# Kernel optimization log

Measured on AMD Instinct MI355X. Metric: run time of the kernel, lower is better.

Reference implementation:

```python
import jax, jax.numpy as jnp
import numpy as np

EPS = 1e-12  # guard sqrt at zero distance


def setup_inputs() -> dict:
    key = jax.random.key(0)
    k1, k2 = jax.random.split(key)
    B, C, N = 4, 3, 8192
    predict_pc = jax.random.normal(k1, (B, C, N), dtype=jnp.float32)
    gt_pc = jax.random.normal(k2, (B, C, N), dtype=jnp.float32)
    return {"predict_pc": predict_pc, "gt_pc": gt_pc}


def reference(predict_pc, gt_pc):
    # predict_pc: [B, 3, Np], gt_pc: [B, 3, Ng]
    B = gt_pc.shape[0]
    Np = predict_pc.shape[2]
    Ng = gt_pc.shape[2]
    denom = B * (Ng + Np)

    # Pairwise Euclidean distances d[b, n, m] = ||predict[b,:,n] - gt[b,:,m]||
    # via the |p|^2 + |g|^2 - 2 p.g expansion (avoids [B,3,Np,Ng] intermediate).
    p2 = jnp.sum(predict_pc * predict_pc, axis=1)            # [B, Np]
    g2 = jnp.sum(gt_pc * gt_pc, axis=1)                      # [B, Ng]
    dot = jnp.einsum('bcn,bcm->bnm', predict_pc, gt_pc)      # [B, Np, Ng]
    d2 = p2[:, :, None] + g2[:, None, :] - 2.0 * dot         # [B, Np, Ng]
    d = jnp.sqrt(jnp.maximum(d2, EPS))

    # z: for each gt point, distance to nearest predicted point -> min over Np
    z = jnp.min(d, axis=1)   # [B, Ng]
    # z_2: for each predicted point, distance to nearest gt point -> min over Ng
    z2 = jnp.min(d, axis=2)  # [B, Np]

    loss = z.sum() / denom + z2.sum() / denom
    return loss
```

## Files before the change

kernel.cpp:

```cpp
#include <hip/hip_runtime.h>
#include <math.h>


#define B_       4
#define N_       8192
#define THREADS  256
#define RX       4
#define XB       (THREADS * RX)
#define XBLKS    (N_ / XB)
#define YSPLITS  16
#define YCHUNK   (N_ / YSPLITS)
#define NGROUPS  (2 * B_ * XBLKS)
#define POISON   0xAAAAAAAAu


__global__ __launch_bounds__(THREADS)
void chamfer_fused_kernel(const float* __restrict__ P, const float* __restrict__ G,
                          unsigned* __restrict__ mins, unsigned* __restrict__ gcnt,
                          unsigned* __restrict__ fcnt, float* __restrict__ gsum,
                          float* __restrict__ out)
{
    __shared__ float4 ytile[YCHUNK];
    __shared__ float red[THREADS];
    __shared__ unsigned s_ticket;

    const int t      = threadIdx.x;
    const int xblk   = blockIdx.x;
    const int ysplit = blockIdx.y;
    const int bz     = blockIdx.z;
    const int pass   = bz >> 2;
    const int b      = bz & 3;
    const int gid    = bz * XBLKS + xblk;

    const float* Xb = (pass ? G : P) + (size_t)b * 3 * N_;
    const float* Yb = (pass ? P : G) + (size_t)b * 3 * N_;

    const int ybase = ysplit * YCHUNK;
#pragma unroll
    for (int k = 0; k < YCHUNK / THREADS; ++k) {
        const int n = ybase + k * THREADS + t;
        float gx = Yb[n];
        float gy = Yb[N_ + n];
        float gz = Yb[2 * N_ + n];
        ytile[k * THREADS + t] = make_float4(gx, gy, gz, fmaf(gx, gx, fmaf(gy, gy, gz * gz)));
    }

    const int xbase = xblk * XB;
    float m2x[RX], m2y[RX], m2z[RX], p2[RX], mn[RX];
#pragma unroll
    for (int r = 0; r < RX; ++r) {
        const int n = xbase + r * THREADS + t;
        float px = Xb[n];
        float py = Xb[N_ + n];
        float pz = Xb[2 * N_ + n];
        p2[r]  = fmaf(px, px, fmaf(py, py, pz * pz));
        m2x[r] = -2.0f * px;
        m2y[r] = -2.0f * py;
        m2z[r] = -2.0f * pz;
        mn[r]  = 3.4e38f;
    }
    __syncthreads();

#pragma unroll 4
    for (int j = 0; j < YCHUNK; ++j) {
        const float4 g = ytile[j];
#pragma unroll
        for (int r = 0; r < RX; ++r) {
            float s = fmaf(m2z[r], g.z, g.w);
            s = fmaf(m2y[r], g.y, s);
            s = fmaf(m2x[r], g.x, s);
            mn[r] = fminf(mn[r], s);
        }
    }

    unsigned* mybase = mins + (size_t)(pass * B_ + b) * N_ + xbase;
#pragma unroll
    for (int r = 0; r < RX; ++r) {
        float v = fmaxf(mn[r] + p2[r], 1e-12f);
        atomicMin(&mybase[r * THREADS + t], __float_as_uint(v));
    }

    __syncthreads();
    if (t == 0) {
        __threadfence();
        s_ticket = atomicAdd(&gcnt[gid], 1u);
    }
    __syncthreads();
    if (s_ticket != POISON + (unsigned)(YSPLITS - 1)) return;

    __threadfence();
    const uint4* vmin = (const uint4*)(mins + (size_t)(pass * B_ + b) * N_ + xbase);
    uint4 q = vmin[t];
    float a = sqrtf(__uint_as_float(q.x)) + sqrtf(__uint_as_float(q.y))
            + sqrtf(__uint_as_float(q.z)) + sqrtf(__uint_as_float(q.w));
    red[t] = a;
    __syncthreads();
    for (int off = 128; off > 0; off >>= 1) {
        if (t < off) red[t] += red[t + off];
        __syncthreads();
    }
    if (t == 0) {
        gsum[gid] = red[0];
        __threadfence();
        s_ticket = atomicAdd(fcnt, 1u);
    }
    __syncthreads();
    if (s_ticket != POISON + (unsigned)(NGROUPS - 1)) return;

    __threadfence();
    red[t] = (t < NGROUPS) ? gsum[t] : 0.0f;
    __syncthreads();
    for (int off = 128; off > 0; off >>= 1) {
        if (t < off) red[t] += red[t + off];
        __syncthreads();
    }
    if (t == 0) out[0] = red[0] * (1.0f / 65536.0f);
}

extern "C" void kernel_launch(void* const* d_in, const int* in_sizes, int n_in,
                              void* d_out, int out_size, void* d_ws, size_t ws_size,
                              hipStream_t stream)
{
    const float* P = (const float*)d_in[0];
    const float* G = (const float*)d_in[1];
    float* out = (float*)d_out;

    unsigned* w    = (unsigned*)d_ws;
    unsigned* mins = w;
    unsigned* gcnt = w + 65536;
    unsigned* fcnt = w + 65600;
    float*    gsum = (float*)(w + 65664);

    dim3 grid(XBLKS, YSPLITS, 2 * B_);
    chamfer_fused_kernel<<<grid, THREADS, 0, stream>>>(P, G, mins, gcnt, fcnt, gsum, out);
}
```

Baseline: 101.9 us.

## Compute each pairwise distance once for both min directions with 8x8 register tiles

Replaces the two separate passes (pred→gt and gt→pred), which each recomputed the full distance matrix, with a single pass. Each thread now holds an 8x8 register tile and updates both row minima and column minima from the same distance values. Column minima are reduced across threads through shared memory each 128-point chunk and merged into global memory with atomicMin. This halves the FMA work but adds per-chunk shared-memory reductions, barriers and more atomics, and the final sum is serialised per batch.

```diff
diff --git a/kernel.cpp b/kernel.cpp
--- a/kernel.cpp
+++ b/kernel.cpp
@@ -5,12 +5,14 @@
 #define B_       4
 #define N_       8192
 #define THREADS  256
-#define RX       4
-#define XB       (THREADS * RX)
-#define XBLKS    (N_ / XB)
-#define YSPLITS  16
-#define YCHUNK   (N_ / YSPLITS)
-#define NGROUPS  (2 * B_ * XBLKS)
+#define RX       8
+#define RY       8
+#define XB       128
+#define XTILES   (N_ / XB)
+#define YSPL     4
+#define YRANGE   (N_ / YSPL)
+#define YC       128
+#define CHUNKS   (YRANGE / YC)
 #define POISON   0xAAAAAAAAu
 
 
@@ -20,101 +22,133 @@
                           unsigned* __restrict__ fcnt, float* __restrict__ gsum,
                           float* __restrict__ out)
 {
-    __shared__ float4 ytile[YCHUNK];
-    __shared__ float red[THREADS];
+    __shared__ float lred[16 * 129];
     __shared__ unsigned s_ticket;
 
-    const int t      = threadIdx.x;
-    const int xblk   = blockIdx.x;
-    const int ysplit = blockIdx.y;
-    const int bz     = blockIdx.z;
-    const int pass   = bz >> 2;
-    const int b      = bz & 3;
-    const int gid    = bz * XBLKS + xblk;
+    const int t     = threadIdx.x;
+    const int tx    = t & 15;
+    const int ty    = t >> 4;
+    const int xtile = blockIdx.x;
+    const int yspl  = blockIdx.y;
+    const int b     = blockIdx.z;
 
-    const float* Xb = (pass ? G : P) + (size_t)b * 3 * N_;
-    const float* Yb = (pass ? P : G) + (size_t)b * 3 * N_;
+    const float* Xb = P + (size_t)b * 3 * N_;
+    const float* Yb = G + (size_t)b * 3 * N_;
 
-    const int ybase = ysplit * YCHUNK;
+    const int x0 = xtile * XB + tx * RX;
+    float4 xa = *(const float4*)&Xb[x0];
+    float4 xb4 = *(const float4*)&Xb[x0 + 4];
+    float4 ya = *(const float4*)&Xb[N_ + x0];
+    float4 yb4 = *(const float4*)&Xb[N_ + x0 + 4];
+    float4 za = *(const float4*)&Xb[2 * N_ + x0];
+    float4 zb4 = *(const float4*)&Xb[2 * N_ + x0 + 4];
+    float px[RX] = {xa.x, xa.y, xa.z, xa.w, xb4.x, xb4.y, xb4.z, xb4.w};
+    float py[RX] = {ya.x, ya.y, ya.z, ya.w, yb4.x, yb4.y, yb4.z, yb4.w};
+    float pz[RX] = {za.x, za.y, za.z, za.w, zb4.x, zb4.y, zb4.z, zb4.w};
+
+    float m2x[RX], m2y[RX], m2z[RX], p2[RX], mnx[RX];
 #pragma unroll
-    for (int k = 0; k < YCHUNK / THREADS; ++k) {
-        const int n = ybase + k * THREADS + t;
-        float gx = Yb[n];
-        float gy = Yb[N_ + n];
-        float gz = Yb[2 * N_ + n];
-        ytile[k * THREADS + t] = make_float4(gx, gy, gz, fmaf(gx, gx, fmaf(gy, gy, gz * gz)));
+    for (int i = 0; i < RX; ++i) {
+        p2[i]  = fmaf(px[i], px[i], fmaf(py[i], py[i], pz[i] * pz[i]));
+        m2x[i] = -2.0f * px[i];
+        m2y[i] = -2.0f * py[i];
+        m2z[i] = -2.0f * pz[i];
+        mnx[i] = 3.4e38f;
     }
 
-    const int xbase = xblk * XB;
-    float m2x[RX], m2y[RX], m2z[RX], p2[RX], mn[RX];
+    const int ybase = yspl * YRANGE;
+    const float* ybp = Yb + ybase + ty * RY;
+    unsigned* ymin_g = mins + 32768 + (size_t)b * N_ + ybase;
+
+    for (int c = 0; c < CHUNKS; ++c) {
+        const float* yc = ybp + c * YC;
+        float4 ga = *(const float4*)&yc[0];
+        float4 gb = *(const float4*)&yc[4];
+        float4 ha = *(const float4*)&yc[N_];
+        float4 hb = *(const float4*)&yc[N_ + 4];
+        float4 ka = *(const float4*)&yc[2 * N_];
+        float4 kb = *(const float4*)&yc[2 * N_ + 4];
+        float gx[RY] = {ga.x, ga.y, ga.z, ga.w, gb.x, gb.y, gb.z, gb.w};
+        float gy[RY] = {ha.x, ha.y, ha.z, ha.w, hb.x, hb.y, hb.z, hb.w};
+        float gz[RY] = {ka.x, ka.y, ka.z, ka.w, kb.x, kb.y, kb.z, kb.w};
+
 #pragma unroll
-    for (int r = 0; r < RX; ++r) {
-        const int n = xbase + r * THREADS + t;
-        float px = Xb[n];
-        float py = Xb[N_ + n];
-        float pz = Xb[2 * N_ + n];
-        p2[r]  = fmaf(px, px, fmaf(py, py, pz * pz));
-        m2x[r] = -2.0f * px;
-        m2y[r] = -2.0f * py;
-        m2z[r] = -2.0f * pz;
-        mn[r]  = 3.4e38f;
+        for (int q = 0; q < RY; ++q) {
+            float g2 = fmaf(gx[q], gx[q], fmaf(gy[q], gy[q], gz[q] * gz[q]));
+            float w[RX];
+#pragma unroll
+            for (int i = 0; i < RX; ++i) {
+                float s = fmaf(m2x[i], gx[q], g2);
+                s = fmaf(m2y[i], gy[q], s);
+                s = fmaf(m2z[i], gz[q], s);
+                mnx[i] = fminf(mnx[i], s);
+                w[i] = s + p2[i];
+            }
+            float t0 = fminf(fminf(w[0], w[1]), w[2]);
+            float t1 = fminf(fminf(w[3], w[4]), w[5]);
+            float t2 = fminf(fminf(w[6], w[7]), t0);
+            lred[tx * 129 + ty * RY + q] = fminf(t1, t2);
+        }
+        __syncthreads();
+        if (t < YC) {
+            float m = lred[t];
+#pragma unroll
+            for (int k = 1; k < 16; ++k) m = fminf(m, lred[k * 129 + t]);
+            atomicMin(&ymin_g[c * YC + t], __float_as_uint(fmaxf(m, 1e-12f)));
+        }
+        __syncthreads();
+    }
+
+#pragma unroll
+    for (int i = 0; i < RX; ++i)
+        lred[ty * 129 + tx * RX + i] = mnx[i] + p2[i];
+    __syncthreads();
+    if (t < XB) {
+        float m = lred[t];
+#pragma unroll
+        for (int k = 1; k < 16; ++k) m = fminf(m, lred[k * 129 + t]);
+        atomicMin(&mins[(size_t)b * N_ + xtile * XB + t],
+                  __float_as_uint(fmaxf(m, 1e-12f)));
     }
     __syncthreads();
 
-#pragma unroll 4
-    for (int j = 0; j < YCHUNK; ++j) {
-        const float4 g = ytile[j];
-#pragma unroll
-        for (int r = 0; r < RX; ++r) {
-            float s = fmaf(m2z[r], g.z, g.w);
-            s = fmaf(m2y[r], g.y, s);
-            s = fmaf(m2x[r], g.x, s);
-            mn[r] = fminf(mn[r], s);
-        }
-    }
-
-    unsigned* mybase = mins + (size_t)(pass * B_ + b) * N_ + xbase;
-#pragma unroll
-    for (int r = 0; r < RX; ++r) {
-        float v = fmaxf(mn[r] + p2[r], 1e-12f);
-        atomicMin(&mybase[r * THREADS + t], __float_as_uint(v));
-    }
-
-    __syncthreads();
     if (t == 0) {
         __threadfence();
-        s_ticket = atomicAdd(&gcnt[gid], 1u);
+        s_ticket = atomicAdd(&gcnt[b], 1u);
     }
     __syncthreads();
-    if (s_ticket != POISON + (unsigned)(YSPLITS - 1)) return;
+    if (s_ticket != POISON + (unsigned)(XTILES * YSPL - 1)) return;
 
     __threadfence();
-    const uint4* vmin = (const uint4*)(mins + (size_t)(pass * B_ + b) * N_ + xbase);
-    uint4 q = vmin[t];
-    float a = sqrtf(__uint_as_float(q.x)) + sqrtf(__uint_as_float(q.y))
-            + sqrtf(__uint_as_float(q.z)) + sqrtf(__uint_as_float(q.w));
-    red[t] = a;
+    const uint4* vx = (const uint4*)(mins + (size_t)b * N_);
+    const uint4* vy = (const uint4*)(mins + 32768 + (size_t)b * N_);
+    float acc = 0.0f;
+#pragma unroll
+    for (int k = 0; k < N_ / 4 / THREADS; ++k) {
+        uint4 a = vx[k * THREADS + t];
+        uint4 c4 = vy[k * THREADS + t];
+        acc += sqrtf(__uint_as_float(a.x)) + sqrtf(__uint_as_float(a.y))
+             + sqrtf(__uint_as_float(a.z)) + sqrtf(__uint_as_float(a.w))
+             + sqrtf(__uint_as_float(c4.x)) + sqrtf(__uint_as_float(c4.y))
+             + sqrtf(__uint_as_float(c4.z)) + sqrtf(__uint_as_float(c4.w));
+    }
+    lred[t] = acc;
     __syncthreads();
     for (int off = 128; off > 0; off >>= 1) {
-        if (t < off) red[t] += red[t + off];
+        if (t < off) lred[t] += lred[t + off];
         __syncthreads();
     }
     if (t == 0) {
-        gsum[gid] = red[0];
+        gsum[b] = lred[0];
         __threadfence();
         s_ticket = atomicAdd(fcnt, 1u);
     }
     __syncthreads();
-    if (s_ticket != POISON + (unsigned)(NGROUPS - 1)) return;
+    if (s_ticket != POISON + (unsigned)(B_ - 1)) return;
 
     __threadfence();
-    red[t] = (t < NGROUPS) ? gsum[t] : 0.0f;
-    __syncthreads();
-    for (int off = 128; off > 0; off >>= 1) {
-        if (t < off) red[t] += red[t + off];
-        __syncthreads();
-    }
-    if (t == 0) out[0] = red[0] * (1.0f / 65536.0f);
+    if (t == 0)
+        out[0] = (gsum[0] + gsum[1] + gsum[2] + gsum[3]) * (1.0f / 65536.0f);
 }
 
 extern "C" void kernel_launch(void* const* d_in, const int* in_sizes, int n_in,
@@ -131,6 +165,6 @@
     unsigned* fcnt = w + 65600;
     float*    gsum = (float*)(w + 65664);
 
-    dim3 grid(XBLKS, YSPLITS, 2 * B_);
+    dim3 grid(XTILES, YSPL, B_);
     chamfer_fused_kernel<<<grid, THREADS, 0, stream>>>(P, G, mins, gcnt, fcnt, gsum, out);
 }
```

Result: slower. 107.2 us (+5.2%).

## Raise per-thread register tile to 16 points and split Y into 64 chunks

Applied to the files above, without the earlier changes.

Each thread now holds 16 query points instead of 4, and the reference set is split into 64 chunks of 128 points instead of 16 chunks of 512. This raises arithmetic per shared-memory load and changes the grid to 2x64x8 blocks. The completion ticket moves from per x-block to per batch-pass group, so one last block reduces all 8192 minima of its group and a single thread sums the 8 group totals. The shared-memory read is software-prefetched one step ahead. The larger register tile and the launch-bounds occupancy hint risk spills or lower occupancy, and the per-group final reduction is serialized into one block.

```diff
diff --git a/kernel.cpp b/kernel.cpp
--- a/kernel.cpp
+++ b/kernel.cpp
@@ -5,22 +5,23 @@
 #define B_       4
 #define N_       8192
 #define THREADS  256
-#define RX       4
+#define RX       16
 #define XB       (THREADS * RX)
 #define XBLKS    (N_ / XB)
-#define YSPLITS  16
+#define YSPLITS  64
 #define YCHUNK   (N_ / YSPLITS)
-#define NGROUPS  (2 * B_ * XBLKS)
+#define NGROUPS  8
+#define BLKS_PER_GROUP (XBLKS * YSPLITS)
 #define POISON   0xAAAAAAAAu
 
 
-__global__ __launch_bounds__(THREADS)
+__global__ __launch_bounds__(THREADS, 4)
 void chamfer_fused_kernel(const float* __restrict__ P, const float* __restrict__ G,
                           unsigned* __restrict__ mins, unsigned* __restrict__ gcnt,
                           unsigned* __restrict__ fcnt, float* __restrict__ gsum,
                           float* __restrict__ out)
 {
-    __shared__ float4 ytile[YCHUNK];
+    __shared__ float4 ytile[YCHUNK + 4];
     __shared__ float red[THREADS];
     __shared__ unsigned s_ticket;
 
@@ -30,77 +31,81 @@
     const int bz     = blockIdx.z;
     const int pass   = bz >> 2;
     const int b      = bz & 3;
-    const int gid    = bz * XBLKS + xblk;
+    const int grp    = bz;
 
     const float* Xb = (pass ? G : P) + (size_t)b * 3 * N_;
     const float* Yb = (pass ? P : G) + (size_t)b * 3 * N_;
 
-    const int ybase = ysplit * YCHUNK;
-#pragma unroll
-    for (int k = 0; k < YCHUNK / THREADS; ++k) {
-        const int n = ybase + k * THREADS + t;
+    if (t < YCHUNK) {
+        const int n = ysplit * YCHUNK + t;
         float gx = Yb[n];
         float gy = Yb[N_ + n];
         float gz = Yb[2 * N_ + n];
-        ytile[k * THREADS + t] = make_float4(gx, gy, gz, fmaf(gx, gx, fmaf(gy, gy, gz * gz)));
+        ytile[t] = make_float4(gx, gy, gz, fmaf(gx, gx, fmaf(gy, gy, gz * gz)));
     }
 
     const int xbase = xblk * XB;
     float m2x[RX], m2y[RX], m2z[RX], p2[RX], mn[RX];
 #pragma unroll
-    for (int r = 0; r < RX; ++r) {
-        const int n = xbase + r * THREADS + t;
+    for (int i = 0; i < RX; ++i) {
+        const int n = xbase + i * THREADS + t;
         float px = Xb[n];
         float py = Xb[N_ + n];
         float pz = Xb[2 * N_ + n];
-        p2[r]  = fmaf(px, px, fmaf(py, py, pz * pz));
-        m2x[r] = -2.0f * px;
-        m2y[r] = -2.0f * py;
-        m2z[r] = -2.0f * pz;
-        mn[r]  = 3.4e38f;
+        p2[i]  = fmaf(px, px, fmaf(py, py, pz * pz));
+        m2x[i] = -2.0f * px;
+        m2y[i] = -2.0f * py;
+        m2z[i] = -2.0f * pz;
+        mn[i]  = 3.4e38f;
     }
     __syncthreads();
 
-#pragma unroll 4
+    float4 g = ytile[0];
+#pragma unroll 2
     for (int j = 0; j < YCHUNK; ++j) {
-        const float4 g = ytile[j];
+        float4 gn = ytile[j + 1];
 #pragma unroll
-        for (int r = 0; r < RX; ++r) {
-            float s = fmaf(m2z[r], g.z, g.w);
-            s = fmaf(m2y[r], g.y, s);
-            s = fmaf(m2x[r], g.x, s);
-            mn[r] = fminf(mn[r], s);
+        for (int i = 0; i < RX; ++i) {
+            float s = fmaf(m2x[i], g.x, g.w);
+            s = fmaf(m2y[i], g.y, s);
+            s = fmaf(m2z[i], g.z, s);
+            mn[i] = fminf(mn[i], s);
         }
+        g = gn;
     }
 
-    unsigned* mybase = mins + (size_t)(pass * B_ + b) * N_ + xbase;
+    unsigned* mybase = mins + (size_t)grp * N_ + xbase;
 #pragma unroll
-    for (int r = 0; r < RX; ++r) {
-        float v = fmaxf(mn[r] + p2[r], 1e-12f);
-        atomicMin(&mybase[r * THREADS + t], __float_as_uint(v));
+    for (int i = 0; i < RX; ++i) {
+        float v = fmaxf(mn[i] + p2[i], 1e-12f);
+        atomicMin(&mybase[i * THREADS + t], __float_as_uint(v));
     }
 
     __syncthreads();
     if (t == 0) {
         __threadfence();
-        s_ticket = atomicAdd(&gcnt[gid], 1u);
+        s_ticket = atomicAdd(&gcnt[grp], 1u);
     }
     __syncthreads();
-    if (s_ticket != POISON + (unsigned)(YSPLITS - 1)) return;
+    if (s_ticket != POISON + (unsigned)(BLKS_PER_GROUP - 1)) return;
 
     __threadfence();
-    const uint4* vmin = (const uint4*)(mins + (size_t)(pass * B_ + b) * N_ + xbase);
-    uint4 q = vmin[t];
-    float a = sqrtf(__uint_as_float(q.x)) + sqrtf(__uint_as_float(q.y))
-            + sqrtf(__uint_as_float(q.z)) + sqrtf(__uint_as_float(q.w));
-    red[t] = a;
+    const uint4* v = (const uint4*)(mins + (size_t)grp * N_);
+    float acc = 0.0f;
+#pragma unroll
+    for (int k = 0; k < N_ / 4 / THREADS; ++k) {
+        uint4 q = v[k * THREADS + t];
+        acc += sqrtf(__uint_as_float(q.x)) + sqrtf(__uint_as_float(q.y))
+             + sqrtf(__uint_as_float(q.z)) + sqrtf(__uint_as_float(q.w));
+    }
+    red[t] = acc;
     __syncthreads();
     for (int off = 128; off > 0; off >>= 1) {
         if (t < off) red[t] += red[t + off];
         __syncthreads();
     }
     if (t == 0) {
-        gsum[gid] = red[0];
+        gsum[grp] = red[0];
         __threadfence();
         s_ticket = atomicAdd(fcnt, 1u);
     }
@@ -108,13 +113,12 @@
     if (s_ticket != POISON + (unsigned)(NGROUPS - 1)) return;
 
     __threadfence();
-    red[t] = (t < NGROUPS) ? gsum[t] : 0.0f;
-    __syncthreads();
-    for (int off = 128; off > 0; off >>= 1) {
-        if (t < off) red[t] += red[t + off];
-        __syncthreads();
+    if (t == 0) {
+        float s = 0.0f;
+#pragma unroll
+        for (int k = 0; k < NGROUPS; ++k) s += gsum[k];
+        out[0] = s * (1.0f / 65536.0f);
     }
-    if (t == 0) out[0] = red[0] * (1.0f / 65536.0f);
 }
 
 extern "C" void kernel_launch(void* const* d_in, const int* in_sizes, int n_in,
```

Result: slower. 104.5 us (+2.6%).
